# Kernel optimization log

Hardware: AMD Instinct MI355X
Metric: run time of the kernel (lower is better)

The kernel has to match this reference:

```python
import jax, jax.numpy as jnp
import numpy as np

D_MODEL = 1024
D_FEATURE = 64
B, S = 4, 4096


def setup_inputs() -> dict:
    key = jax.random.key(0)
    ks = jax.random.split(key, 9)
    s = 1.0 / np.sqrt(D_MODEL)
    return {
        "queries": jax.random.normal(ks[0], (B, S, D_MODEL), jnp.float32),
        "keys": jax.random.normal(ks[1], (B, S, D_MODEL), jnp.float32),
        "values": jax.random.normal(ks[2], (B, S, D_MODEL), jnp.float32),
        "Wq": jax.random.uniform(ks[3], (D_FEATURE, D_MODEL), jnp.float32, -s, s),
        "bq": jax.random.uniform(ks[4], (D_FEATURE,), jnp.float32, -s, s),
        "Wk": jax.random.uniform(ks[5], (D_FEATURE, D_MODEL), jnp.float32, -s, s),
        "bk": jax.random.uniform(ks[6], (D_FEATURE,), jnp.float32, -s, s),
        "Wv": jax.random.uniform(ks[7], (D_FEATURE, D_MODEL), jnp.float32, -s, s),
        "bv": jax.random.uniform(ks[8], (D_FEATURE,), jnp.float32, -s, s),
    }


def reference(queries, keys, values, Wq, bq, Wk, bk, Wv, bv):
    # Linear projections: x @ W.T + b
    q = jnp.einsum("bsm,fm->bsf", queries, Wq) + bq   # [B,S,Df]
    k = jnp.einsum("bsm,fm->bsf", keys, Wk) + bk
    v = jnp.einsum("bsm,fm->bsf", values, Wv) + bv
    d_k = k.shape[-1]
    # Full NxN score matrix (faithful to the naive bmm implementation)
    attn = jnp.einsum("bqf,bkf->bqk", q, k) / jnp.sqrt(jnp.float32(d_k))
    attn = jax.nn.softmax(attn, axis=2)
    # dropout is identity in eval mode; mask is never forwarded in the original
    out = jnp.einsum("bqk,bkf->bqf", attn, v)  # [B,S,Df]
    return out
```

## Files before the change

### kernel.cpp

```cpp
#include <hip/hip_runtime.h>

#define NB 4
#define SEQ 4096
#define DM 1024
#define DF 64

typedef unsigned short u16;
typedef unsigned int u32;
typedef __attribute__((ext_vector_type(8))) _Float16 half8;
typedef __attribute__((ext_vector_type(8))) unsigned short ushort8;
typedef __attribute__((ext_vector_type(4))) float f32x4;

__device__ __forceinline__ u16 f2h(float f) {
    union { _Float16 h; u16 u; } v; v.h = (_Float16)f; return v.u;
}

#define MFMAH(a, b, c) __builtin_amdgcn_mfma_f32_16x16x32_f16(a, b, c, 0, 0, 0)

__global__ __launch_bounds__(256) void wprep_kernel(
    const float* __restrict__ W0, const float* __restrict__ W1, const float* __restrict__ W2,
    u16* __restrict__ Wh)
{
    int i = blockIdx.x * 256 + threadIdx.x;
    const float* W = (i < 65536) ? W0 : (i < 131072) ? W1 : W2;
    Wh[i] = f2h(W[i & 65535]);
}

#define WSTR 264
__global__ __launch_bounds__(256, 3) void proj7_kernel(
    const float* __restrict__ X0, const float* __restrict__ X1, const float* __restrict__ X2,
    const u16* __restrict__ Wh,
    const float* __restrict__ b0, const float* __restrict__ b1, const float* __restrict__ b2,
    u16* __restrict__ Oall)
{
    __shared__ u16 wlds[64 * WSTR];

    const int t    = threadIdx.x;
    const int w    = t >> 6;
    const int lane = t & 63;
    const int m15  = lane & 15;
    const int quad = lane >> 4;
    const int y    = blockIdx.y;

    const float* X    = (y == 0) ? X0 : (y == 1) ? X1 : X2;
    const float* bias = (y == 0) ? b0 : (y == 1) ? b1 : b2;
    const u16*   wp   = Wh + y * 65536;
    u16*         O    = Oall + (size_t)y * (NB * SEQ * DF);

    const long r0 = (long)blockIdx.x * 64;
    const float* xrow = X + (r0 + 16 * w + m15) * DM;

    const int wr2 = t >> 5;
    const int wc  = (t & 31) * 8;

    f32x4 acc[4];
#pragma unroll
    for (int F = 0; F < 4; ++F) acc[F] = (f32x4){0.f, 0.f, 0.f, 0.f};

    ushort8 wreg[8];
#pragma unroll
    for (int i = 0; i < 8; ++i)
        wreg[i] = *(const ushort8*)(wp + (i * 8 + wr2) * DM + wc);

    for (int c = 0; c < 4; ++c) {
        const int k0 = c * 256;
        __syncthreads();
#pragma unroll
        for (int i = 0; i < 8; ++i)
            *(ushort8*)&wlds[(i * 8 + wr2) * WSTR + wc] = wreg[i];
        __syncthreads();

        if (c + 1 < 4) {
#pragma unroll
            for (int i = 0; i < 8; ++i)
                wreg[i] = *(const ushort8*)(wp + (i * 8 + wr2) * DM + k0 + 256 + wc);
        }

#pragma unroll
        for (int s = 0; s < 8; ++s) {
            const int kk = 32 * s + quad * 8;
            float4 x0 = *(const float4*)(xrow + k0 + kk);
            float4 x1 = *(const float4*)(xrow + k0 + kk + 4);
            half8 a;
            a[0] = (_Float16)x0.x; a[1] = (_Float16)x0.y;
            a[2] = (_Float16)x0.z; a[3] = (_Float16)x0.w;
            a[4] = (_Float16)x1.x; a[5] = (_Float16)x1.y;
            a[6] = (_Float16)x1.z; a[7] = (_Float16)x1.w;
#pragma unroll
            for (int F = 0; F < 4; ++F) {
                half8 b = *(const half8*)&wlds[(16 * F + m15) * WSTR + kk];
                acc[F] = MFMAH(a, b, acc[F]);
            }
        }
    }

#pragma unroll
    for (int F = 0; F < 4; ++F) {
        float bv = bias[16 * F + m15];
#pragma unroll
        for (int r = 0; r < 4; ++r)
            O[(r0 + 16 * w + 4 * quad + r) * DF + 16 * F + m15] = f2h(acc[F][r] + bv);
    }
}

#define KSTR 72

__global__ __launch_bounds__(256) void attn_mfma_kernel(
    const u16* __restrict__ Qg, const u16* __restrict__ Kg, const u16* __restrict__ Vg,
    float* __restrict__ Opart, float* __restrict__ Mp, float* __restrict__ Lp,
    int ntiles, int norm)
{
    __shared__ u16 ks[64 * KSTR];
    __shared__ u16 vt[64 * KSTR];
    __shared__ u16 ps[4][16 * KSTR];

    const int t    = threadIdx.x;
    const int w    = t >> 6;
    const int lane = t & 63;
    const int m15  = lane & 15;
    const int quad = lane >> 4;
    const int b    = blockIdx.y;
    const int z    = blockIdx.z;
    const int q0   = blockIdx.x * 64;

    const u16* qptr = Qg + ((long)(b * SEQ + q0 + 16 * w + m15)) * DF + quad * 8;
    half8 qa0 = *(const half8*)qptr;
    half8 qa1 = *(const half8*)(qptr + 32);

    f32x4 accO[4];
#pragma unroll
    for (int F = 0; F < 4; ++F) accO[F] = (f32x4){0.f, 0.f, 0.f, 0.f};
    float mrow[4] = {-1e30f, -1e30f, -1e30f, -1e30f};
    float lrow[4] = {0.f, 0.f, 0.f, 0.f};

    const long kvbase = ((long)b * SEQ + (long)z * ntiles * 64) * DF;
    const ushort4* kb4 = (const ushort4*)(Kg + kvbase);
    const ushort4* vb4 = (const ushort4*)(Vg + kvbase);

    ushort4 kreg[4], vreg[4];
    const int krow  = t >> 4;
    const int kcol4 = t & 15;
    const int vj0   = (t & 15) * 4;
    const int vf0   = (t >> 4) * 4;
#pragma unroll
    for (int c = 0; c < 4; ++c) {
        kreg[c] = kb4[(krow + 16 * c) * 16 + kcol4];
        vreg[c] = vb4[(vj0 + c) * 16 + (vf0 >> 2)];
    }

    for (int tile = 0; tile < ntiles; ++tile) {
        __syncthreads();
#pragma unroll
        for (int c = 0; c < 4; ++c)
            *(ushort4*)&ks[(krow + 16 * c) * KSTR + kcol4 * 4] = kreg[c];
        {
            ushort4 w0 = {vreg[0].x, vreg[1].x, vreg[2].x, vreg[3].x};
            ushort4 w1 = {vreg[0].y, vreg[1].y, vreg[2].y, vreg[3].y};
            ushort4 w2 = {vreg[0].z, vreg[1].z, vreg[2].z, vreg[3].z};
            ushort4 w3 = {vreg[0].w, vreg[1].w, vreg[2].w, vreg[3].w};
            *(ushort4*)&vt[(vf0 + 0) * KSTR + vj0] = w0;
            *(ushort4*)&vt[(vf0 + 1) * KSTR + vj0] = w1;
            *(ushort4*)&vt[(vf0 + 2) * KSTR + vj0] = w2;
            *(ushort4*)&vt[(vf0 + 3) * KSTR + vj0] = w3;
        }
        __syncthreads();

        if (tile + 1 < ntiles) {
#pragma unroll
            for (int c = 0; c < 4; ++c) {
                kreg[c] = kb4[(tile + 1) * 1024 + (krow + 16 * c) * 16 + kcol4];
                vreg[c] = vb4[(tile + 1) * 1024 + (vj0 + c) * 16 + (vf0 >> 2)];
            }
        }

        f32x4 S[4];
#pragma unroll
        for (int T = 0; T < 4; ++T) {
            const u16* kp = &ks[(16 * T + m15) * KSTR + quad * 8];
            half8 kb0 = *(const half8*)kp;
            half8 kb1 = *(const half8*)(kp + 32);
            S[T] = MFMAH(qa0, kb0, ((f32x4){0.f, 0.f, 0.f, 0.f}));
            S[T] = MFMAH(qa1, kb1, S[T]);
        }

        float mx[4], alpha[4], mn[4], psum[4];
#pragma unroll
        for (int T = 0; T < 4; ++T)
#pragma unroll
            for (int r = 0; r < 4; ++r) S[T][r] *= 0.125f;
#pragma unroll
        for (int r = 0; r < 4; ++r) {
            mx[r] = fmaxf(fmaxf(S[0][r], S[1][r]), fmaxf(S[2][r], S[3][r]));
#pragma unroll
            for (int s = 1; s < 16; s <<= 1) mx[r] = fmaxf(mx[r], __shfl_xor(mx[r], s));
            mn[r] = fmaxf(mrow[r], mx[r]);
            alpha[r] = __expf(mrow[r] - mn[r]);
            mrow[r] = mn[r];
            psum[r] = 0.f;
        }
#pragma unroll
        for (int T = 0; T < 4; ++T)
#pragma unroll
            for (int r = 0; r < 4; ++r) {
                float p = __expf(S[T][r] - mn[r]);
                psum[r] += p;
                ps[w][(4 * quad + r) * KSTR + 16 * T + m15] = f2h(p);
            }
#pragma unroll
        for (int r = 0; r < 4; ++r) {
#pragma unroll
            for (int s = 1; s < 16; s <<= 1) psum[r] += __shfl_xor(psum[r], s);
            lrow[r] = lrow[r] * alpha[r] + psum[r];
        }
#pragma unroll
        for (int F = 0; F < 4; ++F)
#pragma unroll
            for (int r = 0; r < 4; ++r) accO[F][r] *= alpha[r];

        const u16* pp = &ps[w][m15 * KSTR + quad * 8];
        half8 pa0 = *(const half8*)pp;
        half8 pa1 = *(const half8*)(pp + 32);
#pragma unroll
        for (int F = 0; F < 4; ++F) {
            const u16* vp = &vt[(16 * F + m15) * KSTR + quad * 8];
            half8 vb0 = *(const half8*)vp;
            half8 vb1 = *(const half8*)(vp + 32);
            accO[F] = MFMAH(pa0, vb0, accO[F]);
            accO[F] = MFMAH(pa1, vb1, accO[F]);
        }
    }

    const long rowbase = (long)b * SEQ + q0 + 16 * w;
    if (norm) {
        float il[4];
#pragma unroll
        for (int r = 0; r < 4; ++r) il[r] = 1.f / lrow[r];
#pragma unroll
        for (int F = 0; F < 4; ++F)
#pragma unroll
            for (int r = 0; r < 4; ++r)
                Opart[(rowbase + 4 * quad + r) * DF + 16 * F + m15] = accO[F][r] * il[r];
    } else {
        float* Og = Opart + (size_t)z * (NB * SEQ * DF);
#pragma unroll
        for (int F = 0; F < 4; ++F)
#pragma unroll
            for (int r = 0; r < 4; ++r)
                Og[(rowbase + 4 * quad + r) * DF + 16 * F + m15] = accO[F][r];
        if (m15 == 0) {
#pragma unroll
            for (int r = 0; r < 4; ++r) {
                long rg = (long)z * (NB * SEQ) + rowbase + 4 * quad + r;
                Mp[rg] = mrow[r];
                Lp[rg] = lrow[r];
            }
        }
    }
}

__global__ __launch_bounds__(256) void combine_kernel(
    const float* __restrict__ Opart, const float* __restrict__ Mp, const float* __restrict__ Lp,
    float* __restrict__ out, int nsplit)
{
    const int tg  = blockIdx.x * 256 + threadIdx.x;
    const int row = tg >> 2;
    const int f0  = (tg & 3) * 16;

    float m = -1e30f;
    for (int g = 0; g < nsplit; ++g) m = fmaxf(m, Mp[g * (NB * SEQ) + row]);

    float l = 0.f;
    float4 o[4];
#pragma unroll
    for (int i = 0; i < 4; ++i) o[i] = (float4){0.f, 0.f, 0.f, 0.f};

    for (int g = 0; g < nsplit; ++g) {
        float e = __expf(Mp[g * (NB * SEQ) + row] - m);
        l += Lp[g * (NB * SEQ) + row] * e;
        const float* Op = Opart + ((long)g * (NB * SEQ) + row) * DF + f0;
#pragma unroll
        for (int i = 0; i < 4; ++i) {
            float4 v = *(const float4*)(Op + 4 * i);
            o[i].x += v.x * e; o[i].y += v.y * e; o[i].z += v.z * e; o[i].w += v.w * e;
        }
    }
    const float inv = 1.f / l;
#pragma unroll
    for (int i = 0; i < 4; ++i) {
        float4 v = {o[i].x * inv, o[i].y * inv, o[i].z * inv, o[i].w * inv};
        *(float4*)(out + (long)row * DF + f0 + 4 * i) = v;
    }
}

extern "C" void kernel_launch(void* const* d_in, const int* in_sizes, int n_in,
                              void* d_out, int out_size, void* d_ws, size_t ws_size,
                              hipStream_t stream) {
    (void)in_sizes; (void)n_in; (void)out_size;

    const float* X[3]  = { (const float*)d_in[0], (const float*)d_in[1], (const float*)d_in[2] };
    const float* W[3]  = { (const float*)d_in[3], (const float*)d_in[5], (const float*)d_in[7] };
    const float* Bv[3] = { (const float*)d_in[4], (const float*)d_in[6], (const float*)d_in[8] };

    char* wsb = (char*)d_ws;
    const size_t P_BYTES  = (size_t)3 * NB * SEQ * DF * 2;
    const size_t WH_BYTES = (size_t)3 * DF * DM * 2;
    const size_t ML_BYTES = (size_t)4 * NB * SEQ * 4;
    const size_t OP_BYTES = (size_t)NB * SEQ * DF * 4;

    u16*   P   = (u16*)wsb;
    u16*   Wh  = (u16*)(wsb + P_BYTES);
    float* Mp  = (float*)(wsb + P_BYTES + WH_BYTES);
    float* Lp  = (float*)(wsb + P_BYTES + WH_BYTES + ML_BYTES);
    float* Op  = (float*)(wsb + P_BYTES + WH_BYTES + 2 * ML_BYTES);
    const size_t base_need = P_BYTES + WH_BYTES + 2 * ML_BYTES;

    int nsplit = 1;
    if (ws_size >= base_need + 4 * OP_BYTES)      nsplit = 4;
    else if (ws_size >= base_need + 2 * OP_BYTES) nsplit = 2;
    const int ntiles = (SEQ / 64) / nsplit;

    float* out = (float*)d_out;

    wprep_kernel<<<768, 256, 0, stream>>>(W[0], W[1], W[2], Wh);

    dim3 pgrid(NB * SEQ / 64, 3);
    proj7_kernel<<<pgrid, 256, 0, stream>>>(X[0], X[1], X[2], Wh,
                                            Bv[0], Bv[1], Bv[2], P);

    const size_t proj_elems = (size_t)NB * SEQ * DF;
    dim3 agrid(SEQ / 64, NB, nsplit);
    if (nsplit == 1) {
        attn_mfma_kernel<<<agrid, 256, 0, stream>>>(P, P + proj_elems, P + 2 * proj_elems,
                                                    out, Mp, Lp, ntiles, 1);
    } else {
        attn_mfma_kernel<<<agrid, 256, 0, stream>>>(P, P + proj_elems, P + 2 * proj_elems,
                                                    Op, Mp, Lp, ntiles, 0);
        combine_kernel<<<(NB * SEQ * 4) / 256, 256, 0, stream>>>(Op, Mp, Lp, out, nsplit);
    }
}
```

Before: 281.7 us.

## Double-buffer projection GEMM with async global-to-LDS loads of X tiles

Restructures the projection kernel so the fp32 input rows are staged into a double-buffered, XOR-swizzled LDS tile using direct global_load_lds. The weight tile shrinks to 64-wide K chunks, also double-buffered. Loads for the next K step are issued while the MFMAs for the current step run. The aim is to hide global latency on the large X stream and replace strided per-lane global reads with coalesced loads. In exchange it uses more LDS (about 50KB per block), which may reduce occupancy, and it adds more barriers, one per 64-wide K step.

Result: slower. 292.3 us (+3.8%).

```diff
diff --git a/kernel.cpp b/kernel.cpp
--- a/kernel.cpp
+++ b/kernel.cpp
@@ -16,6 +16,12 @@
 }
 
 #define MFMAH(a, b, c) __builtin_amdgcn_mfma_f32_16x16x32_f16(a, b, c, 0, 0, 0)
+
+__device__ __forceinline__ void gload16(const void* g, void* l) {
+    __builtin_amdgcn_global_load_lds(
+        (__attribute__((address_space(1))) const void*)g,
+        (__attribute__((address_space(3))) void*)l, 16, 0, 0);
+}
 
 __global__ __launch_bounds__(256) void wprep_kernel(
     const float* __restrict__ W0, const float* __restrict__ W1, const float* __restrict__ W2,
@@ -26,14 +32,14 @@
     Wh[i] = f2h(W[i & 65535]);
 }
 
-#define WSTR 264
-__global__ __launch_bounds__(256, 3) void proj7_kernel(
+__global__ __launch_bounds__(256, 3) void proj10_kernel(
     const float* __restrict__ X0, const float* __restrict__ X1, const float* __restrict__ X2,
     const u16* __restrict__ Wh,
     const float* __restrict__ b0, const float* __restrict__ b1, const float* __restrict__ b2,
     u16* __restrict__ Oall)
 {
-    __shared__ u16 wlds[64 * WSTR];
+    __shared__ float xsf[2][64 * 64];
+    __shared__ u16   wlds2[2][64 * 72];
 
     const int t    = threadIdx.x;
     const int w    = t >> 6;
@@ -48,50 +54,72 @@
     u16*         O    = Oall + (size_t)y * (NB * SEQ * DF);
 
     const long r0 = (long)blockIdx.x * 64;
-    const float* xrow = X + (r0 + 16 * w + m15) * DM;
-
-    const int wr2 = t >> 5;
-    const int wc  = (t & 31) * 8;
+
+    const int xsl = lane & 15;
+    const int xro = lane >> 4;
+
+    const int wrow1 = t >> 2;
+    const int wcol  = (t & 3) * 16;
+
+    const int xrow64 = (16 * w + m15) * 64;
 
     f32x4 acc[4];
 #pragma unroll
     for (int F = 0; F < 4; ++F) acc[F] = (f32x4){0.f, 0.f, 0.f, 0.f};
 
-    ushort8 wreg[8];
-#pragma unroll
-    for (int i = 0; i < 8; ++i)
-        wreg[i] = *(const ushort8*)(wp + (i * 8 + wr2) * DM + wc);
-
-    for (int c = 0; c < 4; ++c) {
-        const int k0 = c * 256;
+#pragma unroll
+    for (int j = 0; j < 4; ++j) {
+        const int rr = (j * 4 + w) * 4 + xro;
+        gload16(X + (r0 + rr) * DM + ((xsl ^ (rr & 15)) << 2),
+                &xsf[0][(j * 4 + w) * 256]);
+    }
+    {
+        ushort8 wa = *(const ushort8*)(wp + wrow1 * DM + wcol);
+        ushort8 wb = *(const ushort8*)(wp + wrow1 * DM + wcol + 8);
+        *(ushort8*)&wlds2[0][wrow1 * 72 + wcol]     = wa;
+        *(ushort8*)&wlds2[0][wrow1 * 72 + wcol + 8] = wb;
+    }
+    __syncthreads();
+
+    int cur = 0;
+    for (int s = 0; s < 16; ++s) {
+        const int nxt = cur ^ 1;
+        ushort8 wa, wb;
+        if (s + 1 < 16) {
+            const int k1 = 64 * (s + 1);
+#pragma unroll
+            for (int j = 0; j < 4; ++j) {
+                const int rr = (j * 4 + w) * 4 + xro;
+                gload16(X + (r0 + rr) * DM + k1 + ((xsl ^ (rr & 15)) << 2),
+                        &xsf[nxt][(j * 4 + w) * 256]);
+            }
+            wa = *(const ushort8*)(wp + wrow1 * DM + k1 + wcol);
+            wb = *(const ushort8*)(wp + wrow1 * DM + k1 + wcol + 8);
+        }
+
+#pragma unroll
+        for (int sh = 0; sh < 2; ++sh) {
+            const int s0 = 8 * sh + 2 * quad;
+            float4 xa = *(const float4*)&xsf[cur][xrow64 + ((s0 ^ m15) << 2)];
+            float4 xb = *(const float4*)&xsf[cur][xrow64 + (((s0 + 1) ^ m15) << 2)];
+            half8 a;
+            a[0] = (_Float16)xa.x; a[1] = (_Float16)xa.y;
+            a[2] = (_Float16)xa.z; a[3] = (_Float16)xa.w;
+            a[4] = (_Float16)xb.x; a[5] = (_Float16)xb.y;
+            a[6] = (_Float16)xb.z; a[7] = (_Float16)xb.w;
+#pragma unroll
+            for (int F = 0; F < 4; ++F) {
+                half8 b = *(const half8*)&wlds2[cur][(16 * F + m15) * 72 + 32 * sh + 8 * quad];
+                acc[F] = MFMAH(a, b, acc[F]);
+            }
+        }
+
+        if (s + 1 < 16) {
+            *(ushort8*)&wlds2[nxt][wrow1 * 72 + wcol]     = wa;
+            *(ushort8*)&wlds2[nxt][wrow1 * 72 + wcol + 8] = wb;
+        }
         __syncthreads();
-#pragma unroll
-        for (int i = 0; i < 8; ++i)
-            *(ushort8*)&wlds[(i * 8 + wr2) * WSTR + wc] = wreg[i];
-        __syncthreads();
-
-        if (c + 1 < 4) {
-#pragma unroll
-            for (int i = 0; i < 8; ++i)
-                wreg[i] = *(const ushort8*)(wp + (i * 8 + wr2) * DM + k0 + 256 + wc);
-        }
-
-#pragma unroll
-        for (int s = 0; s < 8; ++s) {
-            const int kk = 32 * s + quad * 8;
-            float4 x0 = *(const float4*)(xrow + k0 + kk);
-            float4 x1 = *(const float4*)(xrow + k0 + kk + 4);
-            half8 a;
-            a[0] = (_Float16)x0.x; a[1] = (_Float16)x0.y;
-            a[2] = (_Float16)x0.z; a[3] = (_Float16)x0.w;
-            a[4] = (_Float16)x1.x; a[5] = (_Float16)x1.y;
-            a[6] = (_Float16)x1.z; a[7] = (_Float16)x1.w;
-#pragma unroll
-            for (int F = 0; F < 4; ++F) {
-                half8 b = *(const half8*)&wlds[(16 * F + m15) * WSTR + kk];
-                acc[F] = MFMAH(a, b, acc[F]);
-            }
-        }
+        cur = nxt;
     }
 
 #pragma unroll
@@ -324,8 +352,8 @@
     wprep_kernel<<<768, 256, 0, stream>>>(W[0], W[1], W[2], Wh);
 
     dim3 pgrid(NB * SEQ / 64, 3);
-    proj7_kernel<<<pgrid, 256, 0, stream>>>(X[0], X[1], X[2], Wh,
-                                            Bv[0], Bv[1], Bv[2], P);
+    proj10_kernel<<<pgrid, 256, 0, stream>>>(X[0], X[1], X[2], Wh,
+                                             Bv[0], Bv[1], Bv[2], P);
 
     const size_t proj_elems = (size_t)NB * SEQ * DF;
     dim3 agrid(SEQ / 64, NB, nsplit);
```
